# Optimization experiments

Measured on AMD Instinct MI355X. Metric: run time of the kernel, lower is better.

## Reference

```python
import jax, jax.numpy as jnp
import numpy as np

N = 50000        # num nodes (num_paths)
E = 1_600_000    # num edges (avg degree 32)
W = 64           # window_size -> x feature dim
H = 128          # hidden_dimension
TEMP = 1.0       # temperature


def setup_inputs() -> dict:
    key = jax.random.key(0)
    k = jax.random.split(key, 6)
    x = jax.random.normal(k[0], (N, W), dtype=jnp.float32)
    y = jax.random.normal(k[1], (N,), dtype=jnp.float32)
    edge_index = jax.random.randint(k[2], (2, E), 0, N, dtype=jnp.int32)
    w1 = jax.random.normal(k[3], (2 * W, H), dtype=jnp.float32) / np.sqrt(2 * W)
    b1 = jnp.zeros((H,), dtype=jnp.float32)
    w2 = jax.random.normal(k[4], (H, 1), dtype=jnp.float32) / np.sqrt(H)
    b2 = jnp.zeros((1,), dtype=jnp.float32)
    return {"x": x, "y": y, "edge_index": edge_index,
            "w1": w1, "b1": b1, "w2": w2, "b2": b2}


def reference(x, y, edge_index, w1, b1, w2, b2):
    src, dst = edge_index[0], edge_index[1]
    # edge-wise gather + concat: [E, 2W]
    feat = jnp.concatenate([x[src], x[dst]], axis=1)
    # attention MLP: Linear -> ReLU -> Linear
    h = jax.nn.relu(feat @ w1 + b1)          # [E, H]
    logits = (h @ w2 + b2)[:, 0] / TEMP      # [E]
    # segment softmax over destination nodes (numerically stable)
    m = jax.ops.segment_max(logits, dst, num_segments=N)      # [N]
    e = jnp.exp(logits - m[dst])                               # [E]
    denom = jax.ops.segment_sum(e, dst, num_segments=N)       # [N]
    alpha = e / denom[dst]                                     # [E]
    # weighted scatter-sum aggregation
    y_hat = jax.ops.segment_sum(y[src] * alpha, dst, num_segments=N)  # [N]
    return y_hat, alpha[:, None]
```

## Files before the change

### kernel.cpp

```cpp
#include <hip/hip_runtime.h>

#define QSCALE 44.0f

__device__ __forceinline__ unsigned short f2bf(float f) {
    unsigned u = __float_as_uint(f);
    unsigned r = (u + 0x7fffu + ((u >> 16) & 1u)) >> 16;
    return (unsigned short)r;
}
__device__ __forceinline__ float bfu(unsigned short s) {
    return __uint_as_float(((unsigned)s) << 16);
}

__device__ __forceinline__ float dot4_i8(unsigned ax, unsigned bx, const float* w) {
    float acc = 0.f;
#pragma unroll
    for (int i = 0; i < 4; ++i) {
        int va = (int)(char)(ax >> (8 * i));
        int vb = (int)(char)(bx >> (8 * i));
        acc += w[i] * (float)max(va + vb, 0);
    }
    return acc;
}

__device__ __forceinline__ float edge_dot(const uint4& a, const uint4& b, const float* w2r) {
    float acc;
    acc  = dot4_i8(a.x, b.x, w2r + 0);
    acc += dot4_i8(a.y, b.y, w2r + 4);
    acc += dot4_i8(a.z, b.z, w2r + 8);
    acc += dot4_i8(a.w, b.w, w2r + 12);
    acc += __shfl_xor(acc, 1);
    acc += __shfl_xor(acc, 2);
    acc += __shfl_xor(acc, 4);
    return acc;
}

__device__ __forceinline__ unsigned long long pack_contrib(float ev, float ys) {
    float flo = fminf(ev * 65536.f, 1.0e9f);
    float fhi = fmaxf(fminf(ys * ev * 16384.f, 1.0e9f), -1.0e9f);
    unsigned int qlo = (unsigned int)__float2int_rn(flo);
    int          qhi = __float2int_rn(fhi);
    return ((unsigned long long)(unsigned int)qhi << 32) | (unsigned long long)qlo;
}

__global__ __launch_bounds__(256) void proj_kernel(
    const float* __restrict__ x, const float* __restrict__ w1, const float* __restrict__ b1,
    unsigned char* __restrict__ P, unsigned long long* __restrict__ agg, int N)
{
    __shared__ unsigned short wl[64 * 256];
    __shared__ float xs[32 * 64];
    const int t = threadIdx.x;

    for (int i = t; i < 64 * 256; i += 256) {
        int k = i >> 8, j = i & 255;
        float w = (j < 128) ? w1[k * 128 + j] : w1[(64 + k) * 128 + (j - 128)];
        wl[i] = f2bf(w);
    }

    const int jg = t & 63;
    const int ng = t >> 6;
    const int j0 = jg * 4;

    float bb[4] = {0.f, 0.f, 0.f, 0.f};
    if (j0 < 128) {
#pragma unroll
        for (int c = 0; c < 4; ++c) bb[c] = b1[j0 + c];
    }

    const int ntiles = (N + 31) / 32;
    for (int tile = blockIdx.x; tile < ntiles; tile += gridDim.x) {
        const int n0 = tile * 32;

        __syncthreads();
        if (t < 32) {
            int n = n0 + t;
            if (n < N) agg[n] = 0ull;
        }
        for (int i = t; i < 32 * 64; i += 256) {
            int n = n0 + (i >> 6);
            xs[i] = (n < N) ? x[(size_t)n * 64 + (i & 63)] : 0.f;
        }
        __syncthreads();

        float acc[8][4];
#pragma unroll
        for (int i = 0; i < 8; ++i)
#pragma unroll
            for (int c = 0; c < 4; ++c) acc[i][c] = 0.f;

        for (int k = 0; k < 64; k += 4) {
            float wv[4][4];
#pragma unroll
            for (int kk = 0; kk < 4; ++kk) {
                ushort4 wu = *(const ushort4*)&wl[(k + kk) * 256 + j0];
                wv[kk][0] = bfu(wu.x); wv[kk][1] = bfu(wu.y);
                wv[kk][2] = bfu(wu.z); wv[kk][3] = bfu(wu.w);
            }
#pragma unroll
            for (int i = 0; i < 8; ++i) {
                const float4 xv = *(const float4*)&xs[(ng * 8 + i) * 64 + k];
#pragma unroll
                for (int c = 0; c < 4; ++c)
                    acc[i][c] += xv.x * wv[0][c] + xv.y * wv[1][c] + xv.z * wv[2][c] + xv.w * wv[3][c];
            }
        }

#pragma unroll
        for (int i = 0; i < 8; ++i) {
            int n = n0 + ng * 8 + i;
            if (n < N) {
                unsigned pk = 0;
#pragma unroll
                for (int c = 0; c < 4; ++c) {
                    float v = (acc[i][c] + bb[c]) * QSCALE;
                    int q = __float2int_rn(fminf(fmaxf(v, -127.f), 127.f));
                    pk |= ((unsigned)(q & 0xff)) << (8 * c);
                }
                *(unsigned*)(P + (size_t)n * 256 + j0) = pk;
            }
        }
    }
}

__global__ __launch_bounds__(256) void edge_logit_kernel(
    const unsigned char* __restrict__ P, const int* __restrict__ ei,
    const float* __restrict__ y,
    const float* __restrict__ w2, const float* __restrict__ b2,
    float* __restrict__ elog, unsigned long long* __restrict__ agg, int E)
{
    const int lane = threadIdx.x & 7;
    float w2r[16];
#pragma unroll
    for (int c = 0; c < 16; ++c) w2r[c] = w2[lane * 16 + c] * (1.0f / QSCALE);
    const float b2s = b2[0];

    const int slot = (blockIdx.x * 256 + threadIdx.x) >> 3;
    const int nslots = (gridDim.x * 256) >> 3;
    const int lo16 = lane * 16;

    for (int base = slot * 4; base < E; base += nslots * 4) {
        if (base + 3 < E) {
            const int4 s4 = *(const int4*)&ei[base];
            const int4 d4 = *(const int4*)&ei[E + base];

            const uint4 a0 = *(const uint4*)(P + (size_t)s4.x * 256 + lo16);
            const uint4 b0 = *(const uint4*)(P + (size_t)d4.x * 256 + 128 + lo16);
            const uint4 a1 = *(const uint4*)(P + (size_t)s4.y * 256 + lo16);
            const uint4 b1v = *(const uint4*)(P + (size_t)d4.y * 256 + 128 + lo16);
            const uint4 a2 = *(const uint4*)(P + (size_t)s4.z * 256 + lo16);
            const uint4 b2v = *(const uint4*)(P + (size_t)d4.z * 256 + 128 + lo16);
            const uint4 a3 = *(const uint4*)(P + (size_t)s4.w * 256 + lo16);
            const uint4 b3 = *(const uint4*)(P + (size_t)d4.w * 256 + 128 + lo16);

            const float acc0 = edge_dot(a0, b0, w2r);
            const float acc1 = edge_dot(a1, b1v, w2r);
            const float acc2 = edge_dot(a2, b2v, w2r);
            const float acc3 = edge_dot(a3, b3, w2r);

            if (lane == 0) {
                const float ys0 = y[s4.x];
                const float ys1 = y[s4.y];
                const float ys2 = y[s4.z];
                const float ys3 = y[s4.w];
                const float ev0 = __expf(acc0 + b2s);
                const float ev1 = __expf(acc1 + b2s);
                const float ev2 = __expf(acc2 + b2s);
                const float ev3 = __expf(acc3 + b2s);
                *(float4*)&elog[base] = make_float4(ev0, ev1, ev2, ev3);
                atomicAdd(&agg[d4.x], pack_contrib(ev0, ys0));
                atomicAdd(&agg[d4.y], pack_contrib(ev1, ys1));
                atomicAdd(&agg[d4.z], pack_contrib(ev2, ys2));
                atomicAdd(&agg[d4.w], pack_contrib(ev3, ys3));
            }
        } else {
            for (int e = base; e < E; ++e) {
                const int s = ei[e];
                const int d = ei[E + e];
                const uint4 a = *(const uint4*)(P + (size_t)s * 256 + lo16);
                const uint4 b = *(const uint4*)(P + (size_t)d * 256 + 128 + lo16);
                const float acc = edge_dot(a, b, w2r);
                if (lane == 0) {
                    const float ev = __expf(acc + b2s);
                    elog[e] = ev;
                    atomicAdd(&agg[d], pack_contrib(ev, y[s]));
                }
            }
        }
    }
}

__global__ __launch_bounds__(256) void decode_alpha_kernel(
    const int* __restrict__ ei, const unsigned long long* __restrict__ agg,
    float* __restrict__ elog, float* __restrict__ yhat, int N, int E)
{
    const int gtid = blockIdx.x * 256 + threadIdx.x;
    const int ntot = gridDim.x * 256;

    for (int i = gtid; i < N; i += ntot) {
        unsigned long long v = agg[i];
        unsigned int lo = (unsigned int)(v & 0xffffffffull);
        int          hi = (int)(v >> 32);
        yhat[i] = (lo != 0u) ? 4.0f * (float)hi / (float)lo : 0.f;
    }

    for (int base = gtid * 4; base < E; base += ntot * 4) {
        if (base + 3 < E) {
            const int4 d4 = *(const int4*)&ei[E + base];
            float4 ev4 = *(const float4*)&elog[base];
            const unsigned int l0 = (unsigned int)(agg[d4.x] & 0xffffffffull);
            const unsigned int l1 = (unsigned int)(agg[d4.y] & 0xffffffffull);
            const unsigned int l2 = (unsigned int)(agg[d4.z] & 0xffffffffull);
            const unsigned int l3 = (unsigned int)(agg[d4.w] & 0xffffffffull);
            ev4.x = l0 ? ev4.x * (65536.0f / (float)l0) : 0.f;
            ev4.y = l1 ? ev4.y * (65536.0f / (float)l1) : 0.f;
            ev4.z = l2 ? ev4.z * (65536.0f / (float)l2) : 0.f;
            ev4.w = l3 ? ev4.w * (65536.0f / (float)l3) : 0.f;
            *(float4*)&elog[base] = ev4;
        } else {
            for (int e = base; e < E; ++e) {
                const unsigned int lo = (unsigned int)(agg[ei[E + e]] & 0xffffffffull);
                elog[e] = lo ? elog[e] * (65536.0f / (float)lo) : 0.f;
            }
        }
    }
}

extern "C" void kernel_launch(void* const* d_in, const int* in_sizes, int n_in,
                              void* d_out, int out_size, void* d_ws, size_t ws_size,
                              hipStream_t stream) {
    const float* x  = (const float*)d_in[0];
    const float* y  = (const float*)d_in[1];
    const int*   ei = (const int*)d_in[2];
    const float* w1 = (const float*)d_in[3];
    const float* b1 = (const float*)d_in[4];
    const float* w2 = (const float*)d_in[5];
    const float* b2 = (const float*)d_in[6];

    const int N = in_sizes[1];
    const int E = in_sizes[2] / 2;

    float* out  = (float*)d_out;
    float* yhat = out;
    float* elog = out + N;

    char* ws = (char*)d_ws;
    unsigned char* P = (unsigned char*)ws;
    const size_t Pbytes = (size_t)N * 256;
    unsigned long long* agg = (unsigned long long*)(ws + Pbytes);

    proj_kernel<<<768, 256, 0, stream>>>(x, w1, b1, P, agg, N);
    edge_logit_kernel<<<2048, 256, 0, stream>>>(P, ei, y, w2, b2, elog, agg, E);
    decode_alpha_kernel<<<1600, 256, 0, stream>>>(ei, agg, elog, yhat, N, E);
}
```

Baseline: 208.8 us.

## Enlarge projection tile to 64 nodes with 8 columns per thread

The node-projection kernel now processes 64-node tiles, and each thread computes 8 output columns instead of 4, which doubles register-level reuse of each x row loaded from shared memory. The x tile load is vectorised to float4, and the output is written as a uint2. The grid is sized to one block per tile instead of a fixed 768 persistent blocks, so the 32KB bf16 weight staging is repeated in more blocks. The higher register use (64 accumulators) may lower occupancy.

```diff
diff --git a/kernel.cpp b/kernel.cpp
--- a/kernel.cpp
+++ b/kernel.cpp
@@ -1,6 +1,7 @@
 #include <hip/hip_runtime.h>
 
 #define QSCALE 44.0f
+#define PTILE 64
 
 __device__ __forceinline__ unsigned short f2bf(float f) {
     unsigned u = __float_as_uint(f);
@@ -47,7 +48,7 @@
     unsigned char* __restrict__ P, unsigned long long* __restrict__ agg, int N)
 {
     __shared__ unsigned short wl[64 * 256];
-    __shared__ float xs[32 * 64];
+    __shared__ float xs[PTILE * 64];
     const int t = threadIdx.x;
 
     for (int i = t; i < 64 * 256; i += 256) {
@@ -56,50 +57,57 @@
         wl[i] = f2bf(w);
     }
 
-    const int jg = t & 63;
-    const int ng = t >> 6;
-    const int j0 = jg * 4;
-
-    float bb[4] = {0.f, 0.f, 0.f, 0.f};
+    const int jg = t & 31;
+    const int ng = t >> 5;
+    const int j0 = jg * 8;
+
+    float bb[8];
+#pragma unroll
+    for (int c = 0; c < 8; ++c) bb[c] = 0.f;
     if (j0 < 128) {
 #pragma unroll
-        for (int c = 0; c < 4; ++c) bb[c] = b1[j0 + c];
-    }
-
-    const int ntiles = (N + 31) / 32;
+        for (int c = 0; c < 8; ++c) bb[c] = b1[j0 + c];
+    }
+
+    const int ntiles = (N + PTILE - 1) / PTILE;
     for (int tile = blockIdx.x; tile < ntiles; tile += gridDim.x) {
-        const int n0 = tile * 32;
+        const int n0 = tile * PTILE;
 
         __syncthreads();
-        if (t < 32) {
+        if (t < PTILE) {
             int n = n0 + t;
             if (n < N) agg[n] = 0ull;
         }
-        for (int i = t; i < 32 * 64; i += 256) {
-            int n = n0 + (i >> 6);
-            xs[i] = (n < N) ? x[(size_t)n * 64 + (i & 63)] : 0.f;
+        for (int i4 = t; i4 < PTILE * 16; i4 += 256) {
+            int n = n0 + (i4 >> 4);
+            float4 v = make_float4(0.f, 0.f, 0.f, 0.f);
+            if (n < N) v = *(const float4*)&x[(size_t)n * 64 + (i4 & 15) * 4];
+            *(float4*)&xs[i4 * 4] = v;
         }
         __syncthreads();
 
-        float acc[8][4];
+        float acc[8][8];
 #pragma unroll
         for (int i = 0; i < 8; ++i)
 #pragma unroll
-            for (int c = 0; c < 4; ++c) acc[i][c] = 0.f;
+            for (int c = 0; c < 8; ++c) acc[i][c] = 0.f;
 
         for (int k = 0; k < 64; k += 4) {
-            float wv[4][4];
+            float wv[4][8];
 #pragma unroll
             for (int kk = 0; kk < 4; ++kk) {
-                ushort4 wu = *(const ushort4*)&wl[(k + kk) * 256 + j0];
-                wv[kk][0] = bfu(wu.x); wv[kk][1] = bfu(wu.y);
-                wv[kk][2] = bfu(wu.z); wv[kk][3] = bfu(wu.w);
+                const ushort4 wa = *(const ushort4*)&wl[(k + kk) * 256 + j0];
+                const ushort4 wb = *(const ushort4*)&wl[(k + kk) * 256 + j0 + 4];
+                wv[kk][0] = bfu(wa.x); wv[kk][1] = bfu(wa.y);
+                wv[kk][2] = bfu(wa.z); wv[kk][3] = bfu(wa.w);
+                wv[kk][4] = bfu(wb.x); wv[kk][5] = bfu(wb.y);
+                wv[kk][6] = bfu(wb.z); wv[kk][7] = bfu(wb.w);
             }
 #pragma unroll
             for (int i = 0; i < 8; ++i) {
                 const float4 xv = *(const float4*)&xs[(ng * 8 + i) * 64 + k];
 #pragma unroll
-                for (int c = 0; c < 4; ++c)
+                for (int c = 0; c < 8; ++c)
                     acc[i][c] += xv.x * wv[0][c] + xv.y * wv[1][c] + xv.z * wv[2][c] + xv.w * wv[3][c];
             }
         }
@@ -108,14 +116,20 @@
         for (int i = 0; i < 8; ++i) {
             int n = n0 + ng * 8 + i;
             if (n < N) {
-                unsigned pk = 0;
+                uint2 pk = make_uint2(0u, 0u);
 #pragma unroll
                 for (int c = 0; c < 4; ++c) {
                     float v = (acc[i][c] + bb[c]) * QSCALE;
                     int q = __float2int_rn(fminf(fmaxf(v, -127.f), 127.f));
-                    pk |= ((unsigned)(q & 0xff)) << (8 * c);
+                    pk.x |= ((unsigned)(q & 0xff)) << (8 * c);
                 }
-                *(unsigned*)(P + (size_t)n * 256 + j0) = pk;
+#pragma unroll
+                for (int c = 4; c < 8; ++c) {
+                    float v = (acc[i][c] + bb[c]) * QSCALE;
+                    int q = __float2int_rn(fminf(fmaxf(v, -127.f), 127.f));
+                    pk.y |= ((unsigned)(q & 0xff)) << (8 * (c - 4));
+                }
+                *(uint2*)(P + (size_t)n * 256 + j0) = pk;
             }
         }
     }
@@ -247,7 +261,8 @@
     const size_t Pbytes = (size_t)N * 256;
     unsigned long long* agg = (unsigned long long*)(ws + Pbytes);
 
-    proj_kernel<<<768, 256, 0, stream>>>(x, w1, b1, P, agg, N);
+    const int ptiles = (N + PTILE - 1) / PTILE;
+    proj_kernel<<<ptiles, 256, 0, stream>>>(x, w1, b1, P, agg, N);
     edge_logit_kernel<<<2048, 256, 0, stream>>>(P, ei, y, w2, b2, elog, agg, E);
     decode_alpha_kernel<<<1600, 256, 0, stream>>>(ei, agg, elog, yhat, N, E);
 }
```

After: 208.6 us. Within noise of the previous version (-0.1%).

## Restructure projection kernel: one node per thread, wave-uniform weight reads from global

Applied to the files above, without the earlier changes.

Rewrites the node projection GEMM so each thread computes 32 outputs for both weight halves of one node. Weights are read directly from global with a wave-uniform column offset (readfirstlane), so they become scalar loads, and the bf16 weight staging in shared memory is dropped. x tiles are padded to a 65-float stride to avoid bank conflicts. The grid is sized to N/64 blocks instead of a persistent 768-block loop. This removes the per-block conversion of 64x256 weights into LDS and the bf16 rounding, at the cost of 64 accumulator registers per thread and wider per-thread stores.

```diff
diff --git a/kernel.cpp b/kernel.cpp
--- a/kernel.cpp
+++ b/kernel.cpp
@@ -1,15 +1,6 @@
 #include <hip/hip_runtime.h>
 
 #define QSCALE 44.0f
-
-__device__ __forceinline__ unsigned short f2bf(float f) {
-    unsigned u = __float_as_uint(f);
-    unsigned r = (u + 0x7fffu + ((u >> 16) & 1u)) >> 16;
-    return (unsigned short)r;
-}
-__device__ __forceinline__ float bfu(unsigned short s) {
-    return __uint_as_float(((unsigned)s) << 16);
-}
 
 __device__ __forceinline__ float dot4_i8(unsigned ax, unsigned bx, const float* w) {
     float acc = 0.f;
@@ -42,82 +33,70 @@
     return ((unsigned long long)(unsigned int)qhi << 32) | (unsigned long long)qlo;
 }
 
+__device__ __forceinline__ int q8(float v) {
+    return __float2int_rn(fminf(fmaxf(v * QSCALE, -127.f), 127.f)) & 0xff;
+}
+
 __global__ __launch_bounds__(256) void proj_kernel(
     const float* __restrict__ x, const float* __restrict__ w1, const float* __restrict__ b1,
     unsigned char* __restrict__ P, unsigned long long* __restrict__ agg, int N)
 {
-    __shared__ unsigned short wl[64 * 256];
-    __shared__ float xs[32 * 64];
+    __shared__ float xs[64 * 65];
     const int t = threadIdx.x;
-
-    for (int i = t; i < 64 * 256; i += 256) {
-        int k = i >> 8, j = i & 255;
-        float w = (j < 128) ? w1[k * 128 + j] : w1[(64 + k) * 128 + (j - 128)];
-        wl[i] = f2bf(w);
-    }
-
-    const int jg = t & 63;
-    const int ng = t >> 6;
-    const int j0 = jg * 4;
-
-    float bb[4] = {0.f, 0.f, 0.f, 0.f};
-    if (j0 < 128) {
-#pragma unroll
-        for (int c = 0; c < 4; ++c) bb[c] = b1[j0 + c];
-    }
-
-    const int ntiles = (N + 31) / 32;
-    for (int tile = blockIdx.x; tile < ntiles; tile += gridDim.x) {
-        const int n0 = tile * 32;
-
-        __syncthreads();
-        if (t < 32) {
-            int n = n0 + t;
-            if (n < N) agg[n] = 0ull;
-        }
-        for (int i = t; i < 32 * 64; i += 256) {
-            int n = n0 + (i >> 6);
-            xs[i] = (n < N) ? x[(size_t)n * 64 + (i & 63)] : 0.f;
-        }
-        __syncthreads();
-
-        float acc[8][4];
-#pragma unroll
-        for (int i = 0; i < 8; ++i)
-#pragma unroll
-            for (int c = 0; c < 4; ++c) acc[i][c] = 0.f;
-
-        for (int k = 0; k < 64; k += 4) {
-            float wv[4][4];
-#pragma unroll
-            for (int kk = 0; kk < 4; ++kk) {
-                ushort4 wu = *(const ushort4*)&wl[(k + kk) * 256 + j0];
-                wv[kk][0] = bfu(wu.x); wv[kk][1] = bfu(wu.y);
-                wv[kk][2] = bfu(wu.z); wv[kk][3] = bfu(wu.w);
-            }
-#pragma unroll
-            for (int i = 0; i < 8; ++i) {
-                const float4 xv = *(const float4*)&xs[(ng * 8 + i) * 64 + k];
-#pragma unroll
-                for (int c = 0; c < 4; ++c)
-                    acc[i][c] += xv.x * wv[0][c] + xv.y * wv[1][c] + xv.z * wv[2][c] + xv.w * wv[3][c];
-            }
-        }
-
-#pragma unroll
-        for (int i = 0; i < 8; ++i) {
-            int n = n0 + ng * 8 + i;
-            if (n < N) {
-                unsigned pk = 0;
-#pragma unroll
-                for (int c = 0; c < 4; ++c) {
-                    float v = (acc[i][c] + bb[c]) * QSCALE;
-                    int q = __float2int_rn(fminf(fmaxf(v, -127.f), 127.f));
-                    pk |= ((unsigned)(q & 0xff)) << (8 * c);
-                }
-                *(unsigned*)(P + (size_t)n * 256 + j0) = pk;
-            }
-        }
+    const int nloc = t & 63;
+    const int n = blockIdx.x * 64 + nloc;
+    const int j0 = __builtin_amdgcn_readfirstlane((t >> 6) * 32);
+
+    if (t < 64) {
+        int nn = blockIdx.x * 64 + t;
+        if (nn < N) agg[nn] = 0ull;
+    }
+
+    for (int i4 = t; i4 < 64 * 16; i4 += 256) {
+        const int row = i4 >> 4, c4 = (i4 & 15) * 4;
+        const int nn = blockIdx.x * 64 + row;
+        float4 v = make_float4(0.f, 0.f, 0.f, 0.f);
+        if (nn < N) v = *(const float4*)&x[(size_t)nn * 64 + c4];
+        float* d = &xs[row * 65 + c4];
+        d[0] = v.x; d[1] = v.y; d[2] = v.z; d[3] = v.w;
+    }
+    __syncthreads();
+
+    float accA[32], accB[32];
+#pragma unroll
+    for (int c = 0; c < 32; ++c) { accA[c] = b1[j0 + c]; accB[c] = 0.f; }
+
+    const float* __restrict__ xrow = &xs[nloc * 65];
+    for (int k = 0; k < 64; ++k) {
+        const float xv = xrow[k];
+        const float* __restrict__ wa = w1 + k * 128 + j0;
+        const float* __restrict__ wb = w1 + (64 + k) * 128 + j0;
+#pragma unroll
+        for (int c = 0; c < 32; ++c) {
+            accA[c] = fmaf(xv, wa[c], accA[c]);
+            accB[c] = fmaf(xv, wb[c], accB[c]);
+        }
+    }
+
+    if (n < N) {
+        unsigned dwA[8], dwB[8];
+#pragma unroll
+        for (int d = 0; d < 8; ++d) {
+            dwA[d] = (unsigned)q8(accA[d * 4 + 0])
+                   | ((unsigned)q8(accA[d * 4 + 1]) << 8)
+                   | ((unsigned)q8(accA[d * 4 + 2]) << 16)
+                   | ((unsigned)q8(accA[d * 4 + 3]) << 24);
+            dwB[d] = (unsigned)q8(accB[d * 4 + 0])
+                   | ((unsigned)q8(accB[d * 4 + 1]) << 8)
+                   | ((unsigned)q8(accB[d * 4 + 2]) << 16)
+                   | ((unsigned)q8(accB[d * 4 + 3]) << 24);
+        }
+        unsigned char* pA = P + (size_t)n * 256 + j0;
+        unsigned char* pB = P + (size_t)n * 256 + 128 + j0;
+        *(uint4*)(pA)      = make_uint4(dwA[0], dwA[1], dwA[2], dwA[3]);
+        *(uint4*)(pA + 16) = make_uint4(dwA[4], dwA[5], dwA[6], dwA[7]);
+        *(uint4*)(pB)      = make_uint4(dwB[0], dwB[1], dwB[2], dwB[3]);
+        *(uint4*)(pB + 16) = make_uint4(dwB[4], dwB[5], dwB[6], dwB[7]);
     }
 }
 
@@ -247,7 +226,7 @@
     const size_t Pbytes = (size_t)N * 256;
     unsigned long long* agg = (unsigned long long*)(ws + Pbytes);
 
-    proj_kernel<<<768, 256, 0, stream>>>(x, w1, b1, P, agg, N);
+    proj_kernel<<<(N + 63) / 64, 256, 0, stream>>>(x, w1, b1, P, agg, N);
     edge_logit_kernel<<<2048, 256, 0, stream>>>(P, ei, y, w2, b2, elog, agg, E);
     decode_alpha_kernel<<<1600, 256, 0, stream>>>(ei, agg, elog, yhat, N, E);
 }
```

After: 200.3 us. 1.04x faster.
